# Kernel tuning notes

Hardware: AMD Instinct MI355X
Metric: run time of the kernel (lower is better)

The kernel has to match this reference:

```python
import jax, jax.numpy as jnp
import numpy as np

N_SAMPLE, N_ATOMS, N_TOKENS, N_CHAINS = 4, 8192, 1024, 8
AF3_THR = 1.1  # af3_clash_threshold
COUNT_THR = 100  # total_clash > 100
REL_THR = 0.5    # relative_clash > 0.5


def setup_inputs() -> dict:
    key = jax.random.key(0)
    k1, = jax.random.split(key, 1)
    # coords spread out a bit so clashes are sparse-ish but nonzero
    pred_coordinate = jax.random.normal(k1, (N_SAMPLE, N_ATOMS, 3), dtype=jnp.float32) * 5.0
    # balanced sorted chain assignment per token: guarantees all ids 0..N_CHAINS-1 present
    asym_id = ((jnp.arange(N_TOKENS) * N_CHAINS) // N_TOKENS).astype(jnp.int32)
    # monotone atoms -> tokens map (N_ATOMS // N_TOKENS atoms per token)
    atom_to_token_idx = (jnp.arange(N_ATOMS) // (N_ATOMS // N_TOKENS)).astype(jnp.int32)
    return {
        "pred_coordinate": pred_coordinate,
        "asym_id": asym_id,
        "atom_to_token_idx": atom_to_token_idx,
    }


def reference(pred_coordinate, asym_id, atom_to_token_idx):
    # Per-atom chain id, then one-hot chain membership M: [N_atoms, N_chains]
    atom_chain = asym_id[atom_to_token_idx]
    M = jax.nn.one_hot(atom_chain, N_CHAINS, dtype=pred_coordinate.dtype)
    n_per_chain = M.sum(axis=0)  # [C] atoms per chain

    # Squared pairwise distances via gram expansion (avoids [S,N,N,3] diff tensor)
    sq = jnp.sum(pred_coordinate * pred_coordinate, axis=-1)          # [S, N]
    gram = jnp.einsum('snd,smd->snm', pred_coordinate, pred_coordinate)  # [S, N, N]
    d2 = sq[:, :, None] + sq[:, None, :] - 2.0 * gram                 # [S, N, N]

    # dist < thr  <=>  d2 < thr^2 (both non-negative)
    clash = (d2 < AF3_THR * AF3_THR).astype(pred_coordinate.dtype)

    # counts[s, a, b] = #{(i in chain a, j in chain b) : clash}; two small GEMMs
    counts = jnp.einsum('snm,na,mb->sab', clash, M, M)  # [S, C, C]

    # original only fills strict off-diagonal pairs (i < j, mirrored); diagonal stays 0
    off = 1.0 - jnp.eye(N_CHAINS, dtype=counts.dtype)
    total = counts * off
    min_n = jnp.minimum(n_per_chain[:, None], n_per_chain[None, :])
    rel = total / min_n

    af3_clash_details = jnp.stack([total, rel], axis=-1)  # [S, C, C, 2]
    has_af3_clash = (total > COUNT_THR) | (rel > REL_THR)  # [S, C, C] bool
    return has_af3_clash, af3_clash_details
```

## Files before the change

kernel.cpp:

```cpp
#include <hip/hip_runtime.h>

#define NS 4
#define NA 8192
#define NTOK 1024
#define NC 8
#define THREADS 256
#define JSLOTS 4
#define JPB (THREADS * JSLOTS)
#define TI 64
#define TPJ (JPB / TI)
#define GRIDX 448



__global__ __launch_bounds__(THREADS)
void setup_kernel(const float* __restrict__ coords, const int* __restrict__ asym,
                  const int* __restrict__ a2t, float4* __restrict__ staged,
                  int* __restrict__ chain, int* __restrict__ counts) {
  const float THR2 = 1.21f;
  int idx = blockIdx.x * THREADS + threadIdx.x;
  float x = coords[3 * idx + 0], y = coords[3 * idx + 1], z = coords[3 * idx + 2];
  staged[idx] = make_float4(2.0f * x, 2.0f * y, 2.0f * z,
                            2.0f * (THR2 - (x * x + y * y + z * z)));
  if (idx < NA) chain[idx] = asym[a2t[idx]];
  if (idx < NS * NC * NC) counts[idx] = 0;
}

__global__ __launch_bounds__(THREADS, 8)
void clash_kernel(const float4* __restrict__ staged, const int* __restrict__ chain,
                  int* __restrict__ counts) {
  __shared__ int red[NC * NC];

  const int tid = threadIdx.x;
  const int s = blockIdx.z;

  int f = blockIdx.x, jb = 1;
  while (f >= 8 * jb * (jb + 1)) ++jb;
  const int ib = f - 8 * jb * (jb - 1);

  if (tid < NC * NC) red[tid] = 0;

  const float4* __restrict__ sb = staged + (size_t)s * NA;
  const float TWO_THR2 = 2.42f;

  float xj[JSLOTS], yj[JSLOTS], zj[JSLOTS], tj2[JSLOTS];
  int bj[JSLOTS];
#pragma unroll
  for (int u = 0; u < JSLOTS; ++u) {
    int j = jb * JPB + u * THREADS + tid;
    float4 cj = sb[j];
    xj[u] = cj.x; yj[u] = cj.y; zj[u] = cj.z;
    tj2[u] = TWO_THR2 - cj.w;
    bj[u] = chain[j];
  }

  int myi = chain[ib * TI + (tid & 63)];
  const int A = __builtin_amdgcn_readfirstlane(myi);
  bool uniform = __all(myi == A);

  int b0[JSLOTS];
#pragma unroll
  for (int u = 0; u < JSLOTS; ++u) {
    b0[u] = __builtin_amdgcn_readfirstlane(bj[u]);
    uniform = uniform && __all(bj[u] == b0[u]);
  }

  __syncthreads();

  const float4* __restrict__ tg = sb + ib * TI;

  if (uniform) {
    int acc[JSLOTS] = {0, 0, 0, 0};
#pragma unroll 8
    for (int t = 0; t < TI; ++t) {
      float4 ci = tg[t];
#pragma unroll
      for (int u = 0; u < JSLOTS; ++u) {
        float d = fmaf(ci.x, xj[u], fmaf(ci.y, yj[u], fmaf(ci.z, zj[u], ci.w)));
        acc[u] += __popcll(__ballot(d > tj2[u]));
      }
    }
    if ((tid & 63) == 0) {
#pragma unroll
      for (int u = 0; u < JSLOTS; ++u) {
        if (acc[u]) {
          atomicAdd(&red[A * NC + b0[u]], acc[u]);
          atomicAdd(&red[b0[u] * NC + A], acc[u]);
        }
      }
    }
  } else {
    for (int t = 0; t < TI; ++t) {
      float4 ci = tg[t];
      int a = chain[ib * TI + t];
#pragma unroll
      for (int u = 0; u < JSLOTS; ++u) {
        float d = fmaf(ci.x, xj[u], fmaf(ci.y, yj[u], fmaf(ci.z, zj[u], ci.w)));
        if (d > tj2[u]) {
          atomicAdd(&red[a * NC + bj[u]], 1);
          atomicAdd(&red[bj[u] * NC + a], 1);
        }
      }
    }
  }

  __syncthreads();
  if (tid < NC * NC) {
    int v = red[tid];
    if (v) atomicAdd(&counts[s * NC * NC + tid], v);
  }
}

__global__ __launch_bounds__(THREADS)
void finalize_kernel(const int* __restrict__ asym, const int* __restrict__ counts,
                     float* __restrict__ out) {
  __shared__ int hist[NC];
  int tid = threadIdx.x;
  if (tid < NC) hist[tid] = 0;
  __syncthreads();
  for (int t = tid; t < NTOK; t += THREADS) atomicAdd(&hist[asym[t]], NA / NTOK);
  __syncthreads();

  int c = counts[tid];
  int a = (tid >> 3) & 7, b = tid & 7;
  float total = (a == b) ? 0.0f : (float)c;
  float minn = (float)min(hist[a], hist[b]);
  float rel = total / minn;
  out[tid] = ((total > 100.0f) || (rel > 0.5f)) ? 1.0f : 0.0f;
  out[256 + 2 * tid + 0] = total;
  out[256 + 2 * tid + 1] = rel;
}

extern "C" void kernel_launch(void* const* d_in, const int* in_sizes, int n_in,
                              void* d_out, int out_size, void* d_ws, size_t ws_size,
                              hipStream_t stream) {
  const float* coords = (const float*)d_in[0];
  const int* asym = (const int*)d_in[1];
  const int* a2t = (const int*)d_in[2];
  float* out = (float*)d_out;

  float4* staged = (float4*)d_ws;
  int* chain = (int*)(staged + NS * NA);
  int* counts = chain + NA;

  setup_kernel<<<dim3(NS * NA / THREADS), THREADS, 0, stream>>>(coords, asym, a2t,
                                                                staged, chain, counts);
  clash_kernel<<<dim3(GRIDX, 1, NS), THREADS, 0, stream>>>(staged, chain, counts);
  finalize_kernel<<<1, THREADS, 0, stream>>>(asym, counts, out);
}
```

Measured before the change: 77.55 us.

## Fuse setup into clash kernel and stage i-tile in shared memory

Removes the separate setup kernel that precomputed scaled coordinates and per-atom chain ids; the clash kernel now reads raw coordinates, computes the scaled terms itself, and looks up chain ids via the two-level gather. The i-tile is built once per block into shared memory instead of being read from global memory on each iteration. Counts are zeroed with a memset rather than inside a kernel. This saves one kernel launch and the staged buffer round trip. In exchange, j-side loads become strided 3-float reads and redundant gathers, occupancy drops from 8 to 7, and a memset node is added.

```diff
diff --git a/kernel.cpp b/kernel.cpp
--- a/kernel.cpp
+++ b/kernel.cpp
@@ -13,26 +13,16 @@
 
 
 
-__global__ __launch_bounds__(THREADS)
-void setup_kernel(const float* __restrict__ coords, const int* __restrict__ asym,
-                  const int* __restrict__ a2t, float4* __restrict__ staged,
-                  int* __restrict__ chain, int* __restrict__ counts) {
-  const float THR2 = 1.21f;
-  int idx = blockIdx.x * THREADS + threadIdx.x;
-  float x = coords[3 * idx + 0], y = coords[3 * idx + 1], z = coords[3 * idx + 2];
-  staged[idx] = make_float4(2.0f * x, 2.0f * y, 2.0f * z,
-                            2.0f * (THR2 - (x * x + y * y + z * z)));
-  if (idx < NA) chain[idx] = asym[a2t[idx]];
-  if (idx < NS * NC * NC) counts[idx] = 0;
-}
-
-__global__ __launch_bounds__(THREADS, 8)
-void clash_kernel(const float4* __restrict__ staged, const int* __restrict__ chain,
-                  int* __restrict__ counts) {
+__global__ __launch_bounds__(THREADS, 7)
+void clash_kernel(const float* __restrict__ coords, const int* __restrict__ asym,
+                  const int* __restrict__ a2t, int* __restrict__ counts) {
   __shared__ int red[NC * NC];
+  __shared__ float4 itile[TI];
 
   const int tid = threadIdx.x;
   const int s = blockIdx.z;
+  const float THR2 = 1.21f;
+  const float TWO_THR2 = 2.42f;
 
   int f = blockIdx.x, jb = 1;
   while (f >= 8 * jb * (jb + 1)) ++jb;
@@ -40,21 +30,28 @@
 
   if (tid < NC * NC) red[tid] = 0;
 
-  const float4* __restrict__ sb = staged + (size_t)s * NA;
-  const float TWO_THR2 = 2.42f;
+  const float* __restrict__ cb = coords + (size_t)s * NA * 3;
 
   float xj[JSLOTS], yj[JSLOTS], zj[JSLOTS], tj2[JSLOTS];
   int bj[JSLOTS];
 #pragma unroll
   for (int u = 0; u < JSLOTS; ++u) {
     int j = jb * JPB + u * THREADS + tid;
-    float4 cj = sb[j];
-    xj[u] = cj.x; yj[u] = cj.y; zj[u] = cj.z;
-    tj2[u] = TWO_THR2 - cj.w;
-    bj[u] = chain[j];
+    float x = cb[3 * j + 0], y = cb[3 * j + 1], z = cb[3 * j + 2];
+    xj[u] = x + x; yj[u] = y + y; zj[u] = z + z;
+    float sq = fmaf(x, x, fmaf(y, y, z * z));
+    tj2[u] = sq + sq;
+    bj[u] = asym[a2t[j]];
   }
 
-  int myi = chain[ib * TI + (tid & 63)];
+  if (tid < TI) {
+    int i = ib * TI + tid;
+    float x = cb[3 * i + 0], y = cb[3 * i + 1], z = cb[3 * i + 2];
+    float sq = fmaf(x, x, fmaf(y, y, z * z));
+    itile[tid] = make_float4(x + x, y + y, z + z, TWO_THR2 - (sq + sq));
+  }
+
+  int myi = asym[a2t[ib * TI + (tid & 63)]];
   const int A = __builtin_amdgcn_readfirstlane(myi);
   bool uniform = __all(myi == A);
 
@@ -67,13 +64,11 @@
 
   __syncthreads();
 
-  const float4* __restrict__ tg = sb + ib * TI;
-
   if (uniform) {
     int acc[JSLOTS] = {0, 0, 0, 0};
 #pragma unroll 8
     for (int t = 0; t < TI; ++t) {
-      float4 ci = tg[t];
+      float4 ci = itile[t];
 #pragma unroll
       for (int u = 0; u < JSLOTS; ++u) {
         float d = fmaf(ci.x, xj[u], fmaf(ci.y, yj[u], fmaf(ci.z, zj[u], ci.w)));
@@ -91,8 +86,8 @@
     }
   } else {
     for (int t = 0; t < TI; ++t) {
-      float4 ci = tg[t];
-      int a = chain[ib * TI + t];
+      float4 ci = itile[t];
+      int a = asym[a2t[ib * TI + t]];
 #pragma unroll
       for (int u = 0; u < JSLOTS; ++u) {
         float d = fmaf(ci.x, xj[u], fmaf(ci.y, yj[u], fmaf(ci.z, zj[u], ci.w)));
@@ -139,12 +134,9 @@
   const int* a2t = (const int*)d_in[2];
   float* out = (float*)d_out;
 
-  float4* staged = (float4*)d_ws;
-  int* chain = (int*)(staged + NS * NA);
-  int* counts = chain + NA;
+  int* counts = (int*)d_ws;
 
-  setup_kernel<<<dim3(NS * NA / THREADS), THREADS, 0, stream>>>(coords, asym, a2t,
-                                                                staged, chain, counts);
-  clash_kernel<<<dim3(GRIDX, 1, NS), THREADS, 0, stream>>>(staged, chain, counts);
+  hipMemsetAsync(counts, 0, NS * NC * NC * sizeof(int), stream);
+  clash_kernel<<<dim3(GRIDX, 1, NS), THREADS, 0, stream>>>(coords, asym, a2t, counts);
   finalize_kernel<<<1, THREADS, 0, stream>>>(asym, counts, out);
 }
```

Measured after the change: 77.72 us. Within noise of the previous version (+0.2%).
